# Optimization experiments

Measured on AMD Instinct MI355X. Metric: run time of the kernel, lower is better.

## Reference

```python
import jax, jax.numpy as jnp
import numpy as np

B, A, G = 16, 262144, 128


def _make_boxes(key, shape):
    # boxes in (x1, y1, x2, y2) with strictly positive width/height
    k1, k2 = jax.random.split(key)
    cxy = jax.random.uniform(k1, shape[:-1] + (2,), minval=0.0, maxval=1024.0)
    wh = jax.random.uniform(k2, shape[:-1] + (2,), minval=8.0, maxval=256.0)
    return jnp.concatenate([cxy - 0.5 * wh, cxy + 0.5 * wh], axis=-1).astype(jnp.float32)


def setup_inputs() -> dict:
    key = jax.random.key(0)
    k1, k2, k3, k4 = jax.random.split(key, 4)
    bbox_regression = jax.random.normal(k1, (B, A, 4), dtype=jnp.float32)
    anchors = _make_boxes(k2, (A, 4))
    gt_boxes = _make_boxes(k3, (B, G, 4))
    # values in [-2, G): negatives are background/ignored, >=0 index into gt_boxes
    matched_idxs = jax.random.randint(k4, (B, A), -2, G, dtype=jnp.int32)
    return {
        "bbox_regression": bbox_regression,
        "anchors": anchors,
        "gt_boxes": gt_boxes,
        "matched_idxs": matched_idxs,
    }


def _encode(gt, anchors):
    # torchvision BoxCoder.encode_single with weights (1, 1, 1, 1)
    ex_w = anchors[..., 2] - anchors[..., 0]
    ex_h = anchors[..., 3] - anchors[..., 1]
    ex_cx = anchors[..., 0] + 0.5 * ex_w
    ex_cy = anchors[..., 1] + 0.5 * ex_h
    gt_w = gt[..., 2] - gt[..., 0]
    gt_h = gt[..., 3] - gt[..., 1]
    gt_cx = gt[..., 0] + 0.5 * gt_w
    gt_cy = gt[..., 1] + 0.5 * gt_h
    dx = (gt_cx - ex_cx) / ex_w
    dy = (gt_cy - ex_cy) / ex_h
    dw = jnp.log(gt_w / ex_w)
    dh = jnp.log(gt_h / ex_h)
    return jnp.stack([dx, dy, dw, dh], axis=-1)


def reference(bbox_regression, anchors, gt_boxes, matched_idxs):
    fg = matched_idxs >= 0                                  # [B, A] foreground mask
    idx = jnp.maximum(matched_idxs, 0)                      # clamp for safe gather
    matched_gt = jnp.take_along_axis(gt_boxes, idx[..., None], axis=1)  # [B, A, 4]
    target_regression = _encode(matched_gt, anchors[None, :, :])        # [B, A, 4]
    l1 = jnp.sum(jnp.abs(bbox_regression - target_regression), axis=-1)  # [B, A]
    l1 = jnp.where(fg, l1, 0.0)
    num_fg = jnp.sum(fg, axis=1)                            # [B]
    per_image = jnp.sum(l1, axis=1) / jnp.maximum(1, num_fg).astype(l1.dtype)
    return jnp.sum(per_image) / max(1, B)
```

## Files before the change

kernel.cpp:

```cpp
#include <hip/hip_runtime.h>
#include <math.h>

#define BB 16
#define AA 262144
#define GG 128
#define TPB 256
#define NBLK (AA / TPB)


__global__ __launch_bounds__(TPB, 4) void loss_main_kernel(
    const float4* __restrict__ reg,
    const float4* __restrict__ anc,
    const float4* __restrict__ gt,
    const int*   __restrict__ mi,
    float* __restrict__ ws_sum,
    float* __restrict__ ws_cnt)
{
    __shared__ float4 gts[BB * GG];
    __shared__ float redS[BB * 4];
    __shared__ float redC[BB * 4];

    const int t  = threadIdx.x;
    const int bx = blockIdx.x;

#pragma unroll
    for (int i = 0; i < (BB * GG) / TPB; ++i) {
        const float4 g = gt[i * TPB + t];
        const float w = g.z - g.x;
        const float h = g.w - g.y;
        gts[i * TPB + t] = make_float4(g.x + 0.5f * w, g.y + 0.5f * h,
                                       __logf(w), __logf(h));
    }

    const int a = bx * TPB + t;
    const float4 an = anc[a];
    const float ex_w  = an.z - an.x;
    const float ex_h  = an.w - an.y;
    const float ex_cx = an.x + 0.5f * ex_w;
    const float ex_cy = an.y + 0.5f * ex_h;
    const float inv_w = 1.0f / ex_w;
    const float inv_h = 1.0f / ex_h;
    const float lw    = __logf(ex_w);
    const float lh    = __logf(ex_h);

    int mjv[BB];
#pragma unroll
    for (int b = 0; b < BB; ++b) mjv[b] = mi[b * AA + a];

    __syncthreads();

    const int wv   = t >> 6;
    const int lane = t & 63;

#pragma unroll
    for (int half = 0; half < 2; ++half) {
        float4 r[8];
#pragma unroll
        for (int j = 0; j < 8; ++j)
            r[j] = reg[(half * 8 + j) * AA + a];

#pragma unroll
        for (int j = 0; j < 8; ++j) {
            const int b  = half * 8 + j;
            const int mj = mjv[b];
            const float4 g = gts[b * GG + (mj < 0 ? 0 : mj)];

            const float dx = (g.x - ex_cx) * inv_w;
            const float dy = (g.y - ex_cy) * inv_h;
            const float dw = g.z - lw;
            const float dh = g.w - lh;

            const float l1 = fabsf(r[j].x - dx) + fabsf(r[j].y - dy) +
                             fabsf(r[j].z - dw) + fabsf(r[j].w - dh);
            float s = (mj >= 0) ? l1 : 0.0f;

            const unsigned long long bal = __ballot(mj >= 0);
#pragma unroll
            for (int o = 32; o > 0; o >>= 1) s += __shfl_down(s, o);

            if (lane == 0) {
                redS[b * 4 + wv] = s;
                redC[b * 4 + wv] = (float)__popcll(bal);
            }
        }
    }
    __syncthreads();

    if (t < BB) {
        const float s = redS[t * 4] + redS[t * 4 + 1] +
                        redS[t * 4 + 2] + redS[t * 4 + 3];
        const float c = redC[t * 4] + redC[t * 4 + 1] +
                        redC[t * 4 + 2] + redC[t * 4 + 3];
        ws_sum[t * NBLK + bx] = s;
        ws_cnt[t * NBLK + bx] = c;
    }
}

__global__ __launch_bounds__(TPB) void reduce_final_kernel(
    const float* __restrict__ ws_sum,
    const float* __restrict__ ws_cnt,
    float* __restrict__ out)
{
    __shared__ float per_img[BB];
    const int t    = threadIdx.x;
    const int wv   = t >> 6;
    const int lane = t & 63;

#pragma unroll
    for (int k = 0; k < 4; ++k) {
        const int b = wv * 4 + k;
        float s = 0.0f, c = 0.0f;
#pragma unroll
        for (int i = 0; i < NBLK / 64; ++i) {
            s += ws_sum[b * NBLK + i * 64 + lane];
            c += ws_cnt[b * NBLK + i * 64 + lane];
        }
#pragma unroll
        for (int o = 32; o > 0; o >>= 1) {
            s += __shfl_down(s, o);
            c += __shfl_down(c, o);
        }
        if (lane == 0) per_img[b] = s / fmaxf(1.0f, c);
    }
    __syncthreads();

    if (t == 0) {
        float acc = 0.0f;
#pragma unroll
        for (int b = 0; b < BB; ++b) acc += per_img[b];
        out[0] = acc / (float)BB;
    }
}

extern "C" void kernel_launch(void* const* d_in, const int* in_sizes, int n_in,
                              void* d_out, int out_size, void* d_ws, size_t ws_size,
                              hipStream_t stream) {
    const float4* reg = (const float4*)d_in[0];
    const float4* anc = (const float4*)d_in[1];
    const float4* gt  = (const float4*)d_in[2];
    const int*    mi  = (const int*)d_in[3];

    float* ws_sum = (float*)d_ws;
    float* ws_cnt = ws_sum + BB * NBLK;

    loss_main_kernel<<<NBLK, TPB, 0, stream>>>(reg, anc, gt, mi, ws_sum, ws_cnt);
    reduce_final_kernel<<<1, TPB, 0, stream>>>(ws_sum, ws_cnt, (float*)d_out);
}
```

Baseline: 111.0 us.

## Split batch images across a second grid dimension to increase block-level parallelism

The main kernel now launches a 2D grid where each block handles 8 of the 16 images for its anchor tile, instead of all 16. The regression and index loads for the block's images are all issued up front before the sync, so more memory requests are in flight per thread. The gt table in shared memory is halved, the per-block reduction covers 8 images, and the min-occupancy launch bound is dropped. In exchange, anchor loads and anchor-side log/reciprocal work are duplicated across the two block rows.

```diff
diff --git a/kernel.cpp b/kernel.cpp
--- a/kernel.cpp
+++ b/kernel.cpp
@@ -6,9 +6,10 @@
 #define GG 128
 #define TPB 256
 #define NBLK (AA / TPB)
+#define IPB 8
 
 
-__global__ __launch_bounds__(TPB, 4) void loss_main_kernel(
+__global__ __launch_bounds__(TPB) void loss_main_kernel(
     const float4* __restrict__ reg,
     const float4* __restrict__ anc,
     const float4* __restrict__ gt,
@@ -16,16 +17,18 @@
     float* __restrict__ ws_sum,
     float* __restrict__ ws_cnt)
 {
-    __shared__ float4 gts[BB * GG];
-    __shared__ float redS[BB * 4];
-    __shared__ float redC[BB * 4];
+    __shared__ float4 gts[IPB * GG];
+    __shared__ float redS[IPB * 4];
+    __shared__ float redC[IPB * 4];
 
-    const int t  = threadIdx.x;
-    const int bx = blockIdx.x;
+    const int t    = threadIdx.x;
+    const int bx   = blockIdx.x;
+    const int half = blockIdx.y;
+    const int b0   = half * IPB;
 
 #pragma unroll
-    for (int i = 0; i < (BB * GG) / TPB; ++i) {
-        const float4 g = gt[i * TPB + t];
+    for (int i = 0; i < (IPB * GG) / TPB; ++i) {
+        const float4 g = gt[b0 * GG + i * TPB + t];
         const float w = g.z - g.x;
         const float h = g.w - g.y;
         gts[i * TPB + t] = make_float4(g.x + 0.5f * w, g.y + 0.5f * h,
@@ -43,9 +46,12 @@
     const float lw    = __logf(ex_w);
     const float lh    = __logf(ex_h);
 
-    int mjv[BB];
+    int    mjv[IPB];
+    float4 r[IPB];
 #pragma unroll
-    for (int b = 0; b < BB; ++b) mjv[b] = mi[b * AA + a];
+    for (int j = 0; j < IPB; ++j) mjv[j] = mi[(b0 + j) * AA + a];
+#pragma unroll
+    for (int j = 0; j < IPB; ++j) r[j] = reg[(b0 + j) * AA + a];
 
     __syncthreads();
 
@@ -53,46 +59,37 @@
     const int lane = t & 63;
 
 #pragma unroll
-    for (int half = 0; half < 2; ++half) {
-        float4 r[8];
+    for (int j = 0; j < IPB; ++j) {
+        const int mj = mjv[j];
+        const float4 g = gts[j * GG + (mj < 0 ? 0 : mj)];
+
+        const float dx = (g.x - ex_cx) * inv_w;
+        const float dy = (g.y - ex_cy) * inv_h;
+        const float dw = g.z - lw;
+        const float dh = g.w - lh;
+
+        const float l1 = fabsf(r[j].x - dx) + fabsf(r[j].y - dy) +
+                         fabsf(r[j].z - dw) + fabsf(r[j].w - dh);
+        float s = (mj >= 0) ? l1 : 0.0f;
+
+        const unsigned long long bal = __ballot(mj >= 0);
 #pragma unroll
-        for (int j = 0; j < 8; ++j)
-            r[j] = reg[(half * 8 + j) * AA + a];
+        for (int o = 32; o > 0; o >>= 1) s += __shfl_down(s, o);
 
-#pragma unroll
-        for (int j = 0; j < 8; ++j) {
-            const int b  = half * 8 + j;
-            const int mj = mjv[b];
-            const float4 g = gts[b * GG + (mj < 0 ? 0 : mj)];
-
-            const float dx = (g.x - ex_cx) * inv_w;
-            const float dy = (g.y - ex_cy) * inv_h;
-            const float dw = g.z - lw;
-            const float dh = g.w - lh;
-
-            const float l1 = fabsf(r[j].x - dx) + fabsf(r[j].y - dy) +
-                             fabsf(r[j].z - dw) + fabsf(r[j].w - dh);
-            float s = (mj >= 0) ? l1 : 0.0f;
-
-            const unsigned long long bal = __ballot(mj >= 0);
-#pragma unroll
-            for (int o = 32; o > 0; o >>= 1) s += __shfl_down(s, o);
-
-            if (lane == 0) {
-                redS[b * 4 + wv] = s;
-                redC[b * 4 + wv] = (float)__popcll(bal);
-            }
+        if (lane == 0) {
+            redS[j * 4 + wv] = s;
+            redC[j * 4 + wv] = (float)__popcll(bal);
         }
     }
     __syncthreads();
 
-    if (t < BB) {
+    if (t < IPB) {
         const float s = redS[t * 4] + redS[t * 4 + 1] +
                         redS[t * 4 + 2] + redS[t * 4 + 3];
         const float c = redC[t * 4] + redC[t * 4 + 1] +
                         redC[t * 4 + 2] + redC[t * 4 + 3];
-        ws_sum[t * NBLK + bx] = s;
-        ws_cnt[t * NBLK + bx] = c;
+        ws_sum[(b0 + t) * NBLK + bx] = s;
+        ws_cnt[(b0 + t) * NBLK + bx] = c;
     }
 }
 
@@ -143,6 +140,7 @@
     float* ws_sum = (float*)d_ws;
     float* ws_cnt = ws_sum + BB * NBLK;
 
-    loss_main_kernel<<<NBLK, TPB, 0, stream>>>(reg, anc, gt, mi, ws_sum, ws_cnt);
+    dim3 grid(NBLK, BB / IPB);
+    loss_main_kernel<<<grid, TPB, 0, stream>>>(reg, anc, gt, mi, ws_sum, ws_cnt);
     reduce_final_kernel<<<1, TPB, 0, stream>>>(ws_sum, ws_cnt, (float*)d_out);
 }
```

Result: no change. 112.8 us (+1.6%).
